# Kernel optimization log

Hardware: AMD Instinct MI355X
Metric: run time of the kernel (lower is better)

## Reference

```python
import jax, jax.numpy as jnp
import numpy as np

N_LAYERS = 2
IN_DIM = 512
HID = 1024
OUT_DIM = 512
B, T = 64, 256


def lstm_layer(x, W_ih, W_hh, b):
    """Single LSTM layer, batch_first x:[B,T,Din] -> (ys:[B,T,H], h_last:[B,H]).
    PyTorch gate order: i, f, g, o."""
    Bsz = x.shape[0]
    H = W_hh.shape[1]
    # Precompute input projection for all timesteps: [B,T,4H]
    x_proj = jnp.einsum('bti,gi->btg', x, W_ih) + b
    x_proj_t = jnp.swapaxes(x_proj, 0, 1)  # [T,B,4H]

    def step(carry, xt):
        h, c = carry
        gates = xt + h @ W_hh.T  # [B,4H]
        i, f, g, o = jnp.split(gates, 4, axis=-1)
        i = jax.nn.sigmoid(i)
        f = jax.nn.sigmoid(f)
        g = jnp.tanh(g)
        o = jax.nn.sigmoid(o)
        c = f * c + i * g
        h = o * jnp.tanh(c)
        return (h, c), h

    h0 = jnp.zeros((Bsz, H), dtype=x.dtype)
    c0 = jnp.zeros((Bsz, H), dtype=x.dtype)
    (h_last, _), ys = jax.lax.scan(step, (h0, c0), x_proj_t)
    return jnp.swapaxes(ys, 0, 1), h_last


def setup_inputs() -> dict:
    key = jax.random.key(0)
    ks = jax.random.split(key, 12)
    s_ih0 = 1.0 / np.sqrt(HID)
    inp = {
        'x': jax.random.normal(ks[0], (B, T, IN_DIM), dtype=jnp.float32),
        'W_ih0': jax.random.uniform(ks[1], (4 * HID, IN_DIM), minval=-s_ih0, maxval=s_ih0),
        'W_hh0': jax.random.uniform(ks[2], (4 * HID, HID), minval=-s_ih0, maxval=s_ih0),
        'b0': jax.random.uniform(ks[3], (4 * HID,), minval=-s_ih0, maxval=s_ih0),
        'W_ih1': jax.random.uniform(ks[4], (4 * HID, HID), minval=-s_ih0, maxval=s_ih0),
        'W_hh1': jax.random.uniform(ks[5], (4 * HID, HID), minval=-s_ih0, maxval=s_ih0),
        'b1': jax.random.uniform(ks[6], (4 * HID,), minval=-s_ih0, maxval=s_ih0),
        'W_fc': jax.random.uniform(ks[7], (OUT_DIM, HID), minval=-s_ih0, maxval=s_ih0),
        'b_fc': jax.random.uniform(ks[8], (OUT_DIM,), minval=-s_ih0, maxval=s_ih0),
    }
    return inp


def reference(x, W_ih0, W_hh0, b0, W_ih1, W_hh1, b1, W_fc, b_fc):
    ys0, _ = lstm_layer(x, W_ih0, W_hh0, b0)        # [B,T,H]
    _, h_last = lstm_layer(ys0, W_ih1, W_hh1, b1)   # [B,H] == tmp[:, -1, :]
    return h_last @ W_fc.T + b_fc                    # [B,OUT_DIM]
```

## Files before the change

kernel.cpp:

```cpp
#include <hip/hip_runtime.h>
#include <math.h>

#define BATCH 64
#define TT 256
#define IN_DIM 512
#define H 1024
#define SLOT 65536
#define XSLOT 32768

typedef __attribute__((ext_vector_type(8))) _Float16 f16x8;
typedef __attribute__((ext_vector_type(4))) float f32x4;
typedef unsigned int u32;
typedef unsigned long long u64;

#define MFMA16 __builtin_amdgcn_mfma_f32_16x16x32_f16
#define SCOPE_AGENT __HIP_MEMORY_SCOPE_AGENT

union FB { u32 u[4]; f16x8 v; };

__device__ __forceinline__ float sigm(float v) { return 1.f / (1.f + __expf(-v)); }
__device__ __forceinline__ float tanhf_(float v) {
    float e = __expf(-2.f * fabsf(v));
    float r = (1.f - e) / (1.f + e);
    return v < 0.f ? -r : r;
}
__device__ __forceinline__ u32 packu(float v) {
    float s = v * 32.f;
    _Float16 hi = (_Float16)s;
    _Float16 lo = (_Float16)(s - (float)hi);
    return (u32)__builtin_bit_cast(unsigned short, hi)
         | ((u32)__builtin_bit_cast(unsigned short, lo) << 16);
}
__device__ __forceinline__ void unpack8(const u64* r, f16x8& bh, f16x8& bl) {
    FB Hf, Lf;
#pragma unroll
    for (int i = 0; i < 4; ++i) {
        u32 p0 = (u32)r[i], p1 = (u32)(r[i] >> 32);
        Hf.u[i] = __builtin_amdgcn_perm(p1, p0, 0x05040100u);
        Lf.u[i] = __builtin_amdgcn_perm(p1, p0, 0x07060302u);
    }
    bh = Hf.v; bl = Lf.v;
}
__device__ __forceinline__ void wsplit8(const float4& a0, const float4& a1, f16x8& hi, f16x8& lo) {
    float tmp[8] = {a0.x, a0.y, a0.z, a0.w, a1.x, a1.y, a1.z, a1.w};
#pragma unroll
    for (int e = 0; e < 8; ++e) {
        float s = tmp[e] * 64.f;
        _Float16 h_ = (_Float16)s;
        hi[e] = h_;
        lo[e] = (_Float16)(s - (float)h_);
    }
}

__global__ void zero_kernel(u32* __restrict__ p, int n) {
    int i = blockIdx.x * 256 + threadIdx.x;
    if (i < n) p[i] = 0u;
}

__global__ __launch_bounds__(512) void xT_kernel(
    const float* __restrict__ x, u32* __restrict__ xpack) {
    const int tid = threadIdx.x, t = blockIdx.x;
    const int b = tid & 63, kq = tid >> 6;
#pragma unroll
    for (int kb = 0; kb < 8; ++kb) {
        int k = kb * 64 + kq * 8;
        const float* src = x + ((size_t)b * TT + t) * IN_DIM + k;
        float4 v0 = *(const float4*)src;
        float4 v1 = *(const float4*)(src + 4);
        u32 o[8] = {packu(v0.x), packu(v0.y), packu(v0.z), packu(v0.w),
                    packu(v1.x), packu(v1.y), packu(v1.z), packu(v1.w)};
        u32* dst = xpack + (size_t)t * XSLOT + (kb * 8 + kq) * 512 + b * 8;
        *(uint4*)dst = make_uint4(o[0], o[1], o[2], o[3]);
        *(uint4*)(dst + 4) = make_uint4(o[4], o[5], o[6], o[7]);
    }
}

template<int NC, int KX, int XS, int DEP>
__device__ __forceinline__ void rec_body(
    const float* __restrict__ Wih, const float* __restrict__ Whh,
    const float* __restrict__ bias, const u32* __restrict__ xbuf,
    u32* hbuf, int* ownflags, int* depflags,
    float (*scr)[32][66], u32* hx, int gbid) {
    const int tid = threadIdx.x;
    const int l = tid & 63, w = tid >> 6;
    const int arow = l & 15, akg = l >> 4;
    const int eb = l;
    const int KC = NC * 32;

    f16x8 Ah[2][NC], Al[2][NC];
#pragma unroll
    for (int m = 0; m < 2; ++m) {
        const int rp = gbid * 32 + m * 16 + arow;
        const float* wihrow = Wih + (size_t)((rp & 3) * H + (rp >> 2)) * KX;
        const float* whhrow = Whh + (size_t)((rp & 3) * H + (rp >> 2)) * H;
#pragma unroll
        for (int c = 0; c < NC; ++c) {
            int g = w * KC + c * 32 + akg * 8;
            const float* src = (g < KX) ? (wihrow + g) : (whhrow + (g - KX));
            float4 v0 = *(const float4*)src;
            float4 v1 = *(const float4*)(src + 4);
            wsplit8(v0, v1, Ah[m][c], Al[m][c]);
        }
    }
#pragma unroll
    for (int m = 0; m < 2; ++m)
#pragma unroll
        for (int c = 0; c < NC; ++c)
            asm volatile("" : "+a"(Ah[m][c]), "+a"(Al[m][c]));

    int boff[NC];
    bool bh_[NC];
#pragma unroll
    for (int c = 0; c < NC; ++c) {
        int g0 = w * KC + c * 32;
        bool ish = (g0 >= KX);
        int gl = ish ? (g0 - KX) : g0;
        boff[c] = (gl >> 3) * 512 + akg * 512 + arow * 8;
        bh_[c] = ish;
    }
    float gbias[4];
#pragma unroll
    for (int g = 0; g < 4; ++g) {
        int rp = gbid * 32 + w * 4 + g;
        gbias[g] = bias[(rp & 3) * H + (rp >> 2)];
    }

    float cs = 0.f;

    for (int t = 0; t < TT; ++t) {
        if (DEP || t > 0) {
            if (w == 0) {
                bool done = false;
                while (!done) {
                    int o0 = __hip_atomic_load(&ownflags[l], __ATOMIC_RELAXED, SCOPE_AGENT);
                    int o1 = __hip_atomic_load(&ownflags[l + 64], __ATOMIC_RELAXED, SCOPE_AGENT);
                    bool ok = ((o0 < o1 ? o0 : o1) >= t);
                    if (DEP) {
                        int d0 = __hip_atomic_load(&depflags[l], __ATOMIC_RELAXED, SCOPE_AGENT);
                        int d1 = __hip_atomic_load(&depflags[l + 64], __ATOMIC_RELAXED, SCOPE_AGENT);
                        ok = ok && ((d0 < d1 ? d0 : d1) >= t + 1);
                    }
                    done = __all(ok);
                    if (!done) __builtin_amdgcn_s_sleep(1);
                }
            }
            __builtin_amdgcn_sched_barrier(0);
            __syncthreads();
        }

        const u32* xb = xbuf + (size_t)(DEP ? t + 1 : t) * XS;
        const u32* hb = hbuf + (size_t)t * SLOT;

        f32x4 acc[2][4];
#pragma unroll
        for (int m = 0; m < 2; ++m)
#pragma unroll
            for (int ns = 0; ns < 4; ++ns) acc[m][ns] = (f32x4){0.f, 0.f, 0.f, 0.f};

#pragma unroll
        for (int c = 0; c < NC; ++c) {
            const u32* bp0 = (bh_[c] ? hb : xb) + boff[c];
            u64 raw[4][4];
#pragma unroll
            for (int ns = 0; ns < 4; ++ns) {
                const u32* bp = bp0 + ns * 128;
                *(uint4*)&raw[ns][0] = *(const uint4*)bp;
                *(uint4*)&raw[ns][2] = *(const uint4*)(bp + 4);
            }
#pragma unroll
            for (int ns = 0; ns < 4; ++ns) {
                f16x8 bh, bl;
                unpack8(raw[ns], bh, bl);
#pragma unroll
                for (int m = 0; m < 2; ++m) {
                    acc[m][ns] = MFMA16(Ah[m][c], bh, acc[m][ns], 0, 0, 0);
                    acc[m][ns] = MFMA16(Ah[m][c], bl, acc[m][ns], 0, 0, 0);
                    acc[m][ns] = MFMA16(Al[m][c], bh, acc[m][ns], 0, 0, 0);
                }
            }
        }
#pragma unroll
        for (int m = 0; m < 2; ++m)
#pragma unroll
            for (int ns = 0; ns < 4; ++ns)
#pragma unroll
                for (int r = 0; r < 4; ++r)
                    scr[w][m * 16 + akg * 4 + r][ns * 16 + arow] = acc[m][ns][r];
        __syncthreads();

        {
            float gg[4];
#pragma unroll
            for (int g = 0; g < 4; ++g) {
                int rl = w * 4 + g;
                float s = 0.f;
#pragma unroll
                for (int ww = 0; ww < 8; ++ww) s += scr[ww][rl][eb];
                gg[g] = s * (1.f / 2048.f) + gbias[g];
            }
            float is = sigm(gg[0]), fs = sigm(gg[1]), gt = tanhf_(gg[2]), os = sigm(gg[3]);
            cs = fs * cs + is * gt;
            float hnew = os * tanhf_(cs);
            hx[w * 72 + eb] = packu(hnew);
        }
        __syncthreads();

        {
            u32 pko = hx[(tid & 7) * 72 + (tid >> 3)];
            __hip_atomic_store(&hbuf[(size_t)(t + 1) * SLOT + gbid * 512 + tid], pko,
                               __ATOMIC_RELAXED, SCOPE_AGENT);
        }
        __syncthreads();
        if (tid == 0)
            __hip_atomic_store(&ownflags[gbid], t + 1, __ATOMIC_RELEASE, SCOPE_AGENT);
    }
}

__global__ __launch_bounds__(512)
__attribute__((amdgpu_waves_per_eu(2, 2)))
void rec_fused(
    const float* __restrict__ Wih0, const float* __restrict__ Whh0, const float* __restrict__ b0,
    const float* __restrict__ Wih1, const float* __restrict__ Whh1, const float* __restrict__ b1,
    const u32* __restrict__ xpack, u32* ys, u32* hs1, int* flags0, int* flags1) {
    __shared__ float scr[8][32][66];
    __shared__ u32 hx[8 * 72];
    const int bid = blockIdx.x;
    if (bid < 128)
        rec_body<6, 512, XSLOT, 0>(Wih0, Whh0, b0, xpack, ys, flags0, nullptr, scr, hx, bid);
    else
        rec_body<8, 1024, SLOT, 1>(Wih1, Whh1, b1, ys, hs1, flags1, flags0, scr, hx, bid - 128);
}

__global__ __launch_bounds__(256) void fc_kernel(
    const u32* __restrict__ hp, const float* __restrict__ Wfc,
    const float* __restrict__ bfc, float* __restrict__ out) {
    const int tid = threadIdx.x;
    const int b = tid & 63;
    const int o = blockIdx.x * 4 + (tid >> 6);
    const float* wr = Wfc + (size_t)o * H;
    float acc = 0.f;
    for (int jb = 0; jb < 128; ++jb) {
        const u64* bp = (const u64*)(hp + (size_t)jb * 512 + b * 8);
        u64 raw[4] = {bp[0], bp[1], bp[2], bp[3]};
        f16x8 vh, vl;
        unpack8(raw, vh, vl);
#pragma unroll
        for (int e = 0; e < 8; ++e) {
            float hv = ((float)vh[e] + (float)vl[e]) * (1.f / 32.f);
            acc += hv * wr[jb * 8 + e];
        }
    }
    out[(size_t)b * 512 + o] = acc + bfc[o];
}

extern "C" void kernel_launch(void* const* d_in, const int* in_sizes, int n_in,
                              void* d_out, int out_size, void* d_ws, size_t ws_size,
                              hipStream_t stream) {
    const float* x    = (const float*)d_in[0];
    const float* Wih0 = (const float*)d_in[1];
    const float* Whh0 = (const float*)d_in[2];
    const float* b0   = (const float*)d_in[3];
    const float* Wih1 = (const float*)d_in[4];
    const float* Whh1 = (const float*)d_in[5];
    const float* b1   = (const float*)d_in[6];
    const float* Wfc  = (const float*)d_in[7];
    const float* bfc  = (const float*)d_in[8];
    float* out = (float*)d_out;

    char* p = (char*)d_ws;
    u32* ys     = (u32*)p; p += (size_t)257 * SLOT * 4;
    u32* hs1    = (u32*)p; p += (size_t)257 * SLOT * 4;
    u32* xpack  = (u32*)p; p += (size_t)256 * XSLOT * 4;
    int* flags0 = (int*)p; p += 512;
    int* flags1 = (int*)p;

    zero_kernel<<<SLOT / 256, 256, 0, stream>>>(ys, SLOT);
    zero_kernel<<<SLOT / 256, 256, 0, stream>>>(hs1, SLOT);
    zero_kernel<<<1, 256, 0, stream>>>((u32*)flags0, 256);

    xT_kernel<<<TT, 512, 0, stream>>>(x, xpack);

    rec_fused<<<256, 512, 0, stream>>>(
        Wih0, Whh0, b0, Wih1, Whh1, b1, xpack, ys, hs1, flags0, flags1);

    fc_kernel<<<128, 256, 0, stream>>>(hs1 + (size_t)256 * SLOT, Wfc, bfc, out);
}
```

Before: 4.329 ms.

## Overlap input-projection MFMAs with recurrent-state wait and vectorize h stores

Reorders the K dimension so every wave owns both input-projection chunks and recurrent chunks, then issues the input-side MFMAs before spinning on the flags of other blocks for h(t). This hides part of the cross-block synchronization latency behind independent work. The h write-back is also changed from per-thread dword atomic stores to 16-byte write-through stores from 128 threads, followed by an explicit vmcnt wait before the release flag. Correctness relies on the sc0 sc1 write-through store being visible at agent scope before the flag is released.

Result: faster. 3.546 ms, median of 3 (-18.1%).

```diff
diff --git a/kernel.cpp b/kernel.cpp
--- a/kernel.cpp
+++ b/kernel.cpp
@@ -12,6 +12,7 @@
 typedef __attribute__((ext_vector_type(4))) float f32x4;
 typedef unsigned int u32;
 typedef unsigned long long u64;
+typedef __attribute__((ext_vector_type(4))) u32 u32x4;
 
 #define MFMA16 __builtin_amdgcn_mfma_f32_16x16x32_f16
 #define SCOPE_AGENT __HIP_MEMORY_SCOPE_AGENT
@@ -50,6 +51,10 @@
         hi[e] = h_;
         lo[e] = (_Float16)(s - (float)h_);
     }
+}
+__device__ __forceinline__ void store16_wt(u32* addr, u32x4 v) {
+    asm volatile("global_store_dwordx4 %0, %1, off sc0 sc1"
+                 :: "v"((u64)(uintptr_t)addr), "v"(v) : "memory");
 }
 
 __global__ void zero_kernel(u32* __restrict__ p, int n) {
@@ -75,7 +80,7 @@
     }
 }
 
-template<int NC, int KX, int XS, int DEP>
+template<int NC, int NCA, int KX, int XS, int DEP>
 __device__ __forceinline__ void rec_body(
     const float* __restrict__ Wih, const float* __restrict__ Whh,
     const float* __restrict__ bias, const u32* __restrict__ xbuf,
@@ -85,7 +90,6 @@
     const int l = tid & 63, w = tid >> 6;
     const int arow = l & 15, akg = l >> 4;
     const int eb = l;
-    const int KC = NC * 32;
 
     f16x8 Ah[2][NC], Al[2][NC];
 #pragma unroll
@@ -95,7 +99,7 @@
         const float* whhrow = Whh + (size_t)((rp & 3) * H + (rp >> 2)) * H;
 #pragma unroll
         for (int c = 0; c < NC; ++c) {
-            int g = w * KC + c * 32 + akg * 8;
+            int g = (c * 8 + w) * 32 + akg * 8;
             const float* src = (g < KX) ? (wihrow + g) : (whhrow + (g - KX));
             float4 v0 = *(const float4*)src;
             float4 v1 = *(const float4*)(src + 4);
@@ -109,14 +113,11 @@
             asm volatile("" : "+a"(Ah[m][c]), "+a"(Al[m][c]));
 
     int boff[NC];
-    bool bh_[NC];
 #pragma unroll
     for (int c = 0; c < NC; ++c) {
-        int g0 = w * KC + c * 32;
-        bool ish = (g0 >= KX);
-        int gl = ish ? (g0 - KX) : g0;
+        int g0 = (c * 8 + w) * 32;
+        int gl = (g0 >= KX) ? (g0 - KX) : g0;
         boff[c] = (gl >> 3) * 512 + akg * 512 + arow * 8;
-        bh_[c] = ish;
     }
     float gbias[4];
 #pragma unroll
@@ -128,38 +129,29 @@
     float cs = 0.f;
 
     for (int t = 0; t < TT; ++t) {
-        if (DEP || t > 0) {
+        f32x4 acc[2][4];
+#pragma unroll
+        for (int m = 0; m < 2; ++m)
+#pragma unroll
+            for (int ns = 0; ns < 4; ++ns) acc[m][ns] = (f32x4){0.f, 0.f, 0.f, 0.f};
+
+        if (DEP) {
             if (w == 0) {
                 bool done = false;
                 while (!done) {
-                    int o0 = __hip_atomic_load(&ownflags[l], __ATOMIC_RELAXED, SCOPE_AGENT);
-                    int o1 = __hip_atomic_load(&ownflags[l + 64], __ATOMIC_RELAXED, SCOPE_AGENT);
-                    bool ok = ((o0 < o1 ? o0 : o1) >= t);
-                    if (DEP) {
-                        int d0 = __hip_atomic_load(&depflags[l], __ATOMIC_RELAXED, SCOPE_AGENT);
-                        int d1 = __hip_atomic_load(&depflags[l + 64], __ATOMIC_RELAXED, SCOPE_AGENT);
-                        ok = ok && ((d0 < d1 ? d0 : d1) >= t + 1);
-                    }
-                    done = __all(ok);
+                    int d0 = __hip_atomic_load(&depflags[l], __ATOMIC_RELAXED, SCOPE_AGENT);
+                    int d1 = __hip_atomic_load(&depflags[l + 64], __ATOMIC_RELAXED, SCOPE_AGENT);
+                    done = __all(((d0 < d1) ? d0 : d1) >= t + 1);
                     if (!done) __builtin_amdgcn_s_sleep(1);
                 }
             }
             __builtin_amdgcn_sched_barrier(0);
             __syncthreads();
         }
-
         const u32* xb = xbuf + (size_t)(DEP ? t + 1 : t) * XS;
-        const u32* hb = hbuf + (size_t)t * SLOT;
-
-        f32x4 acc[2][4];
-#pragma unroll
-        for (int m = 0; m < 2; ++m)
-#pragma unroll
-            for (int ns = 0; ns < 4; ++ns) acc[m][ns] = (f32x4){0.f, 0.f, 0.f, 0.f};
-
-#pragma unroll
-        for (int c = 0; c < NC; ++c) {
-            const u32* bp0 = (bh_[c] ? hb : xb) + boff[c];
+#pragma unroll
+        for (int c = 0; c < NCA; ++c) {
+            const u32* bp0 = xb + boff[c];
             u64 raw[4][4];
 #pragma unroll
             for (int ns = 0; ns < 4; ++ns) {
@@ -179,6 +171,43 @@
                 }
             }
         }
+
+        if (w == 0) {
+            bool done = false;
+            while (!done) {
+                int o0 = __hip_atomic_load(&ownflags[l], __ATOMIC_RELAXED, SCOPE_AGENT);
+                int o1 = __hip_atomic_load(&ownflags[l + 64], __ATOMIC_RELAXED, SCOPE_AGENT);
+                done = __all(((o0 < o1) ? o0 : o1) >= t);
+                if (!done) __builtin_amdgcn_s_sleep(1);
+            }
+        }
+        __builtin_amdgcn_sched_barrier(0);
+        __syncthreads();
+
+        const u32* hb = hbuf + (size_t)t * SLOT;
+#pragma unroll
+        for (int c = NCA; c < NC; ++c) {
+            const u32* bp0 = hb + boff[c];
+            u64 raw[4][4];
+#pragma unroll
+            for (int ns = 0; ns < 4; ++ns) {
+                const u32* bp = bp0 + ns * 128;
+                *(uint4*)&raw[ns][0] = *(const uint4*)bp;
+                *(uint4*)&raw[ns][2] = *(const uint4*)(bp + 4);
+            }
+#pragma unroll
+            for (int ns = 0; ns < 4; ++ns) {
+                f16x8 bh, bl;
+                unpack8(raw[ns], bh, bl);
+#pragma unroll
+                for (int m = 0; m < 2; ++m) {
+                    acc[m][ns] = MFMA16(Ah[m][c], bh, acc[m][ns], 0, 0, 0);
+                    acc[m][ns] = MFMA16(Ah[m][c], bl, acc[m][ns], 0, 0, 0);
+                    acc[m][ns] = MFMA16(Al[m][c], bh, acc[m][ns], 0, 0, 0);
+                }
+            }
+        }
+
 #pragma unroll
         for (int m = 0; m < 2; ++m)
 #pragma unroll
@@ -205,11 +234,16 @@
         }
         __syncthreads();
 
-        {
-            u32 pko = hx[(tid & 7) * 72 + (tid >> 3)];
-            __hip_atomic_store(&hbuf[(size_t)(t + 1) * SLOT + gbid * 512 + tid], pko,
-                               __ATOMIC_RELAXED, SCOPE_AGENT);
-        }
+        if (tid < 128) {
+            int base = tid * 4;
+            u32x4 v;
+            v.x = hx[((base + 0) & 7) * 72 + ((base + 0) >> 3)];
+            v.y = hx[((base + 1) & 7) * 72 + ((base + 1) >> 3)];
+            v.z = hx[((base + 2) & 7) * 72 + ((base + 2) >> 3)];
+            v.w = hx[((base + 3) & 7) * 72 + ((base + 3) >> 3)];
+            store16_wt(hbuf + (size_t)(t + 1) * SLOT + gbid * 512 + base, v);
+        }
+        asm volatile("s_waitcnt vmcnt(0)" ::: "memory");
         __syncthreads();
         if (tid == 0)
             __hip_atomic_store(&ownflags[gbid], t + 1, __ATOMIC_RELEASE, SCOPE_AGENT);
@@ -226,9 +260,9 @@
     __shared__ u32 hx[8 * 72];
     const int bid = blockIdx.x;
     if (bid < 128)
-        rec_body<6, 512, XSLOT, 0>(Wih0, Whh0, b0, xpack, ys, flags0, nullptr, scr, hx, bid);
+        rec_body<6, 2, 512, XSLOT, 0>(Wih0, Whh0, b0, xpack, ys, flags0, nullptr, scr, hx, bid);
     else
-        rec_body<8, 1024, SLOT, 1>(Wih1, Whh1, b1, ys, hs1, flags1, flags0, scr, hx, bid - 128);
+        rec_body<8, 4, 1024, SLOT, 1>(Wih1, Whh1, b1, ys, hs1, flags1, flags0, scr, hx, bid - 128);
 }
 
 __global__ __launch_bounds__(256) void fc_kernel(
```
